# Kernel optimization log

Measured on AMD Instinct MI355X. Metric: run time of the kernel, lower is better.

## Reference

```python
import jax, jax.numpy as jnp
import numpy as np

N = 50000
E = 400000
NFEAT = 256
NHID = 64
HEADS = [4, 4, 4]
NCLASS = 121
NEG_SLOPE = 0.2


def gat_conv(h, W, al, ar, src, dst, H, D):
    # h: [N, F_in], W: [F_in, H*D], al/ar: [H, D]
    feat = (h @ W).reshape(N, H, D)                    # [N, H, D]
    el = jnp.sum(feat * al[None], axis=-1)             # [N, H]
    er = jnp.sum(feat * ar[None], axis=-1)             # [N, H]
    e = jax.nn.leaky_relu(el[src] + er[dst], NEG_SLOPE)  # [E, H]
    # edge softmax over incoming edges of each dst node
    m = jax.ops.segment_max(e, dst, num_segments=N)    # [N, H]
    ex = jnp.exp(e - m[dst])                           # [E, H]
    s = jax.ops.segment_sum(ex, dst, num_segments=N)   # [N, H]
    alpha = ex / s[dst]                                # [E, H]
    msg = alpha[..., None] * feat[src]                 # [E, H, D]
    return jax.ops.segment_sum(msg, dst, num_segments=N)  # [N, H, D]


def setup_inputs() -> dict:
    key = jax.random.key(0)
    ks = jax.random.split(key, 12)
    d = {
        "h": jax.random.normal(ks[0], (N, NFEAT), dtype=jnp.float32),
        "src": jax.random.randint(ks[1], (E,), 0, N),
        "dst": jax.random.randint(ks[2], (E,), 0, N),
        "W1": jax.random.normal(ks[3], (NFEAT, HEADS[0] * NHID), dtype=jnp.float32) * 0.05,
        "al1": jax.random.normal(ks[4], (HEADS[0], NHID), dtype=jnp.float32) * 0.1,
        "ar1": jax.random.normal(ks[5], (HEADS[0], NHID), dtype=jnp.float32) * 0.1,
        "W2": jax.random.normal(ks[6], (HEADS[0] * NHID, HEADS[1] * NHID), dtype=jnp.float32) * 0.05,
        "al2": jax.random.normal(ks[7], (HEADS[1], NHID), dtype=jnp.float32) * 0.1,
        "ar2": jax.random.normal(ks[8], (HEADS[1], NHID), dtype=jnp.float32) * 0.1,
        "W3": jax.random.normal(ks[9], (HEADS[1] * NHID, HEADS[2] * NCLASS), dtype=jnp.float32) * 0.05,
        "al3": jax.random.normal(ks[10], (HEADS[2], NCLASS), dtype=jnp.float32) * 0.1,
        "ar3": jax.random.normal(ks[11], (HEADS[2], NCLASS), dtype=jnp.float32) * 0.1,
    }
    return d


def reference(h, src, dst, W1, al1, ar1, W2, al2, ar2, W3, al3, ar3):
    # layer 1: [N, H0, NHID] -> flatten -> ELU (norm='none', drop=0, residual='none')
    x = gat_conv(h, W1, al1, ar1, src, dst, HEADS[0], NHID).reshape(N, -1)
    x = jax.nn.elu(x)
    # layer 2
    x = gat_conv(x, W2, al2, ar2, src, dst, HEADS[1], NHID).reshape(N, -1)
    x = jax.nn.elu(x)
    # output layer: mean over heads
    x = gat_conv(x, W3, al3, ar3, src, dst, HEADS[2], NCLASS).mean(axis=1)
    return x
```

## Files before the change

kernel.cpp:

```cpp
#include <hip/hip_runtime.h>
#include <cstddef>

#define NN 50000
#define NE 400000
#define NH 4
#define NC 121
#define MAXSLOT 600000

typedef __attribute__((ext_vector_type(8))) short short8;
typedef __attribute__((ext_vector_type(4))) float f32x4;
typedef __attribute__((ext_vector_type(2))) float f32x2;

static __device__ __forceinline__ unsigned short f2bf(float f) {
    unsigned u = __float_as_uint(f);
    u += 0x7fffu + ((u >> 16) & 1u);
    return (unsigned short)(u >> 16);
}
static __device__ __forceinline__ float bf2f(unsigned short u) {
    return __uint_as_float(((unsigned)u) << 16);
}
static __device__ __forceinline__ f32x2 bfpair(unsigned u) {
    f32x2 r;
    r.x = __uint_as_float(u << 16);
    r.y = __uint_as_float(u & 0xffff0000u);
    return r;
}
static __device__ __forceinline__ void load_lds16(const unsigned short* g, unsigned short* l) {
    __builtin_amdgcn_global_load_lds(
        (const __attribute__((address_space(1))) unsigned*)g,
        (__attribute__((address_space(3))) unsigned*)l, 16, 0, 0);
}

#define PREP_X    3200000
#define PREP_BT1  (PREP_X + 65536)
#define PREP_BT2  (PREP_BT1 + 65536)
#define PREP_CAT  (PREP_BT2 + 131072)
#define PREP_WV   (PREP_CAT + 2048)
__global__ __launch_bounds__(256) void prep_k(const float* __restrict__ h,
                                              const float* __restrict__ W1,
                                              const float* __restrict__ W2,
                                              const float* __restrict__ W3,
                                              const float* __restrict__ al3,
                                              const float* __restrict__ ar3,
                                              unsigned short* __restrict__ h_bf,
                                              unsigned short* __restrict__ BT1,
                                              unsigned short* __restrict__ BT2,
                                              unsigned short* __restrict__ BTcat,
                                              float* __restrict__ wl3,
                                              float* __restrict__ wr3) {
    int i = blockIdx.x * blockDim.x + threadIdx.x;
    if (i < PREP_X) {
        float4 v = *(const float4*)&h[(size_t)i * 4];
        ushort4 o;
        o.x = f2bf(v.x); o.y = f2bf(v.y); o.z = f2bf(v.z); o.w = f2bf(v.w);
        *(ushort4*)&h_bf[(size_t)i * 4] = o;
    } else if (i < PREP_BT1) {
        int j = i - PREP_X;
        int n = j >> 8, k = j & 255;
        BT1[j] = f2bf(W1[(size_t)k * 256 + n]);
    } else if (i < PREP_BT2) {
        int j = i - PREP_BT1;
        int n = j >> 8, k = j & 255;
        BT2[j] = f2bf(W2[(size_t)k * 256 + n]);
    } else if (i < PREP_CAT) {
        int j = i - PREP_BT2;
        int c = j >> 10, kk = j & 1023;
        int hh = kk >> 8, k = kk & 255;
        float v = (c < NC) ? 0.25f * W3[(size_t)k * 484 + hh * NC + c] : 0.f;
        BTcat[j] = f2bf(v);
    } else if (i < PREP_WV) {
        int j = (i - PREP_CAT) & 1023;
        int sel = (i - PREP_CAT) >> 10;
        int hh = j >> 8, k = j & 255;
        const float* a = sel ? ar3 : al3;
        const float* wrow = W3 + (size_t)k * 484 + hh * NC;
        const float* arow = a + hh * NC;
        float s = 0.f;
        for (int d = 0; d < NC; ++d) s += wrow[d] * arow[d];
        if (sel) wr3[j] = s; else wl3[j] = s;
    }
}

__global__ __launch_bounds__(256) void gemm_bf16(const unsigned short* __restrict__ A,
                                                 const unsigned short* __restrict__ BT,
                                                 float* __restrict__ Cf,
                                                 unsigned short* __restrict__ Cb,
                                                 const float* __restrict__ al,
                                                 const float* __restrict__ ar,
                                                 float* __restrict__ el,
                                                 float* __restrict__ er,
                                                 int M, int Nout, int K) {
    __shared__ __align__(16) unsigned short Alds[128 * 32];
    __shared__ __align__(16) unsigned short Blds[128 * 32];
    const int tid = threadIdx.x;
    const int wave = tid >> 6;
    const int lane = tid & 63;
    const int quad = lane >> 4;
    const int ml = lane & 15;
    const int m0 = blockIdx.x * 128;
    const int n0 = blockIdx.y * 128;
    const int wm0 = (wave >> 1) * 64;
    const int wn0 = (wave & 1) * 64;

    const unsigned short* Ab = A + (size_t)(m0 + wave * 16 + (lane >> 2)) * K + (lane & 3) * 8;
    const unsigned short* Bb = BT + (size_t)(n0 + wave * 16 + (lane >> 2)) * K + (lane & 3) * 8;
    unsigned short* AldsW = Alds + wave * 512;
    unsigned short* BldsW = Blds + wave * 512;

    f32x4 acc[4][4] = {};

    for (int k0 = 0; k0 < K; k0 += 32) {
        #pragma unroll
        for (int p = 0; p < 2; ++p) {
            load_lds16(Ab + (size_t)(p * 64) * K + k0, AldsW + p * 2048);
            load_lds16(Bb + (size_t)(p * 64) * K + k0, BldsW + p * 2048);
        }
        __syncthreads();

        short8 af[4], bf[4];
        #pragma unroll
        for (int i = 0; i < 4; ++i)
            af[i] = *(const short8*)&Alds[(wm0 + i * 16 + ml) * 32 + quad * 8];
        #pragma unroll
        for (int j = 0; j < 4; ++j)
            bf[j] = *(const short8*)&Blds[(wn0 + j * 16 + ml) * 32 + quad * 8];
        #pragma unroll
        for (int i = 0; i < 4; ++i)
            #pragma unroll
            for (int j = 0; j < 4; ++j)
                acc[i][j] = __builtin_amdgcn_mfma_f32_16x16x32_bf16(af[i], bf[j], acc[i][j], 0, 0, 0);
        __syncthreads();
    }

    #pragma unroll
    for (int i = 0; i < 4; ++i) {
        #pragma unroll
        for (int reg = 0; reg < 4; ++reg) {
            int m = m0 + wm0 + i * 16 + quad * 4 + reg;
            if (m >= M) continue;
            #pragma unroll
            for (int j = 0; j < 4; ++j) {
                int n = n0 + wn0 + j * 16 + ml;
                if (n < Nout) {
                    if (Cb) Cb[(size_t)m * Nout + n] = f2bf(acc[i][j][reg]);
                    else    Cf[(size_t)m * Nout + n] = acc[i][j][reg];
                }
            }
        }
    }

    if (el) {
        int head = (n0 + wn0) >> 6;
        float alv[4], arv[4];
        #pragma unroll
        for (int j = 0; j < 4; ++j) {
            alv[j] = al[head * 64 + j * 16 + ml];
            arv[j] = ar[head * 64 + j * 16 + ml];
        }
        #pragma unroll
        for (int i = 0; i < 4; ++i) {
            #pragma unroll
            for (int reg = 0; reg < 4; ++reg) {
                float sl = 0.f, sr = 0.f;
                #pragma unroll
                for (int j = 0; j < 4; ++j) {
                    float v = acc[i][j][reg];
                    sl += v * alv[j];
                    sr += v * arv[j];
                }
                #pragma unroll
                for (int off = 1; off < 16; off <<= 1) {
                    sl += __shfl_xor(sl, off);
                    sr += __shfl_xor(sr, off);
                }
                int m = m0 + wm0 + i * 16 + quad * 4 + reg;
                if (ml == 0 && m < M) {
                    el[m * 4 + head] = sl;
                    er[m * 4 + head] = sr;
                }
            }
        }
    }
}

__global__ __launch_bounds__(256) void hist_k(const int* __restrict__ dst, int* __restrict__ deg) {
    int e = blockIdx.x * blockDim.x + threadIdx.x;
    if (e < NE) atomicAdd(&deg[dst[e]], 1);
}

__global__ __launch_bounds__(256) void scan1(const int* __restrict__ deg,
                                             int* __restrict__ excl,
                                             int* __restrict__ partials) {
    __shared__ int sh[256];
    int i = blockIdx.x * 256 + threadIdx.x;
    int v = (i < NN) ? ((deg[i] + 3) & ~3) : 0;
    sh[threadIdx.x] = v;
    __syncthreads();
    for (int off = 1; off < 256; off <<= 1) {
        int t = (threadIdx.x >= off) ? sh[threadIdx.x - off] : 0;
        __syncthreads();
        sh[threadIdx.x] += t;
        __syncthreads();
    }
    if (i < NN) excl[i] = sh[threadIdx.x] - v;
    if (threadIdx.x == 255) partials[blockIdx.x] = sh[255];
}

__global__ __launch_bounds__(256) void scan2(int* __restrict__ partials, int nb) {
    __shared__ int sh[256];
    int t = threadIdx.x;
    int v = (t < nb) ? partials[t] : 0;
    sh[t] = v;
    __syncthreads();
    for (int off = 1; off < 256; off <<= 1) {
        int x = (t >= off) ? sh[t - off] : 0;
        __syncthreads();
        sh[t] += x;
        __syncthreads();
    }
    if (t < nb) partials[t] = sh[t] - v;
}

__global__ __launch_bounds__(256) void scan3(const int* __restrict__ excl,
                                             const int* __restrict__ partials,
                                             int* __restrict__ rowptr) {
    int i = blockIdx.x * 256 + threadIdx.x;
    if (i < NN) rowptr[i] = excl[i] + partials[blockIdx.x];
}

__global__ __launch_bounds__(256) void scatter_k(const int* __restrict__ src,
                                                 const int* __restrict__ dst,
                                                 const int* __restrict__ rowptr,
                                                 int* __restrict__ cursor,
                                                 int* __restrict__ ssrc,
                                                 int* __restrict__ sdst) {
    int e = blockIdx.x * blockDim.x + threadIdx.x;
    if (e >= NE) return;
    int d = dst[e];
    int p = atomicAdd(&cursor[d], 1);
    int pos = rowptr[d] + p;
    ssrc[pos] = src[e] << 9;
    sdst[pos] = d;
}

__global__ __launch_bounds__(256) void edgew_k(const int* __restrict__ ssrc,
                                               const int* __restrict__ sdst,
                                               const float* __restrict__ el,
                                               const float* __restrict__ er,
                                               float* __restrict__ wcsr) {
    int i = blockIdx.x * blockDim.x + threadIdx.x;
    if (i >= MAXSLOT) return;
    int d = sdst[i];
    float w0 = 0.f, w1 = 0.f, w2 = 0.f, w3 = 0.f;
    if (d >= 0) {
        int su = ssrc[i];
        float4 e_l = *(const float4*)((const char*)el + (su >> 5));
        float4 e_r = *(const float4*)&er[d * 4];
        float v0 = e_l.x + e_r.x; v0 = fmaxf(v0, 0.2f * v0);
        float v1 = e_l.y + e_r.y; v1 = fmaxf(v1, 0.2f * v1);
        float v2 = e_l.z + e_r.z; v2 = fmaxf(v2, 0.2f * v2);
        float v3 = e_l.w + e_r.w; v3 = fmaxf(v3, 0.2f * v3);
        w0 = __expf(v0); w1 = __expf(v1); w2 = __expf(v2); w3 = __expf(v3);
    }
    wcsr[0 * MAXSLOT + i] = w0;
    wcsr[1 * MAXSLOT + i] = w1;
    wcsr[2 * MAXSLOT + i] = w2;
    wcsr[3 * MAXSLOT + i] = w3;
}

__global__ __launch_bounds__(256) void agg256(const int* __restrict__ rowptr,
                                              const int* __restrict__ deg,
                                              const int* __restrict__ ssrc,
                                              const float* __restrict__ wcsr,
                                              const unsigned short* __restrict__ feat,
                                              unsigned short* __restrict__ ybf,
                                              const float* __restrict__ wl3,
                                              const float* __restrict__ wr3,
                                              float* __restrict__ el3,
                                              float* __restrict__ er3) {
    int wid = (blockIdx.x * blockDim.x + threadIdx.x) >> 6;
    int lane = threadIdx.x & 63;
    if (wid >= NN) return;
    int n = wid;
    int start = rowptr[n];
    int cnt4 = (deg[n] + 3) & ~3;
    int head = lane >> 4;
    const float* wch = wcsr + (size_t)head * MAXSLOT;
    const char* fbase = (const char*)feat + lane * 8;
    f32x2 a01 = {0.f, 0.f}, a23 = {0.f, 0.f};
    float ssum = 0.f;
    for (int k = 0; k < cnt4; k += 4) {
        int4 sv = *(const int4*)&ssrc[start + k];
        float4 w4 = *(const float4*)&wch[start + k];
        uint2 u0 = *(const uint2*)(fbase + sv.x);
        uint2 u1 = *(const uint2*)(fbase + sv.y);
        uint2 u2 = *(const uint2*)(fbase + sv.z);
        uint2 u3 = *(const uint2*)(fbase + sv.w);
        ssum += (w4.x + w4.y) + (w4.z + w4.w);
        a01 += w4.x * bfpair(u0.x); a23 += w4.x * bfpair(u0.y);
        a01 += w4.y * bfpair(u1.x); a23 += w4.y * bfpair(u1.y);
        a01 += w4.z * bfpair(u2.x); a23 += w4.z * bfpair(u2.y);
        a01 += w4.w * bfpair(u3.x); a23 += w4.w * bfpair(u3.y);
    }
    float inv = ssum > 0.f ? 1.0f / ssum : 0.f;
    float r0 = a01.x * inv, r1 = a01.y * inv, r2 = a23.x * inv, r3 = a23.y * inv;
    r0 = r0 > 0.f ? r0 : (__expf(r0) - 1.f);
    r1 = r1 > 0.f ? r1 : (__expf(r1) - 1.f);
    r2 = r2 > 0.f ? r2 : (__expf(r2) - 1.f);
    r3 = r3 > 0.f ? r3 : (__expf(r3) - 1.f);
    ushort4 o;
    o.x = f2bf(r0); o.y = f2bf(r1); o.z = f2bf(r2); o.w = f2bf(r3);
    *(ushort4*)&ybf[(size_t)n * 256 + lane * 4] = o;

    if (wl3) {
        float sl[4], sr[4];
        #pragma unroll
        for (int h = 0; h < 4; ++h) {
            float4 a4 = *(const float4*)&wl3[h * 256 + lane * 4];
            float4 b4 = *(const float4*)&wr3[h * 256 + lane * 4];
            sl[h] = r0 * a4.x + r1 * a4.y + r2 * a4.z + r3 * a4.w;
            sr[h] = r0 * b4.x + r1 * b4.y + r2 * b4.z + r3 * b4.w;
        }
        #pragma unroll
        for (int off = 32; off; off >>= 1) {
            #pragma unroll
            for (int h = 0; h < 4; ++h) {
                sl[h] += __shfl_xor(sl[h], off);
                sr[h] += __shfl_xor(sr[h], off);
            }
        }
        if (lane == 0) {
            #pragma unroll
            for (int h = 0; h < 4; ++h) {
                el3[n * 4 + h] = sl[h];
                er3[n * 4 + h] = sr[h];
            }
        }
    }
}

__global__ __launch_bounds__(256) void agg3(const int* __restrict__ rowptr,
                                            const int* __restrict__ deg,
                                            const int* __restrict__ ssrc,
                                            const float* __restrict__ wcsr,
                                            const unsigned short* __restrict__ x,
                                            unsigned short* __restrict__ xagg) {
    int wid = (blockIdx.x * blockDim.x + threadIdx.x) >> 6;
    int lane = threadIdx.x & 63;
    if (wid >= NN) return;
    int n = wid;
    int start = rowptr[n];
    int cnt4 = (deg[n] + 3) & ~3;
    const char* xbase = (const char*)x + lane * 8;
    f32x2 accA[4] = {}, accB[4] = {};
    float ssum[4] = {};
    for (int k = 0; k < cnt4; k += 4) {
        int4 sv = *(const int4*)&ssrc[start + k];
        float4 w0 = *(const float4*)&wcsr[0 * MAXSLOT + start + k];
        float4 w1 = *(const float4*)&wcsr[1 * MAXSLOT + start + k];
        float4 w2 = *(const float4*)&wcsr[2 * MAXSLOT + start + k];
        float4 w3 = *(const float4*)&wcsr[3 * MAXSLOT + start + k];
        uint2 u0 = *(const uint2*)(xbase + sv.x);
        uint2 u1 = *(const uint2*)(xbase + sv.y);
        uint2 u2 = *(const uint2*)(xbase + sv.z);
        uint2 u3 = *(const uint2*)(xbase + sv.w);
        ssum[0] += (w0.x + w0.y) + (w0.z + w0.w);
        ssum[1] += (w1.x + w1.y) + (w1.z + w1.w);
        ssum[2] += (w2.x + w2.y) + (w2.z + w2.w);
        ssum[3] += (w3.x + w3.y) + (w3.z + w3.w);
        f32x2 fa = bfpair(u0.x), fA = bfpair(u0.y);
        f32x2 fb = bfpair(u1.x), fB = bfpair(u1.y);
        f32x2 fc = bfpair(u2.x), fC = bfpair(u2.y);
        f32x2 fd = bfpair(u3.x), fD = bfpair(u3.y);
        accA[0] += w0.x * fa + w0.y * fb + w0.z * fc + w0.w * fd;
        accB[0] += w0.x * fA + w0.y * fB + w0.z * fC + w0.w * fD;
        accA[1] += w1.x * fa + w1.y * fb + w1.z * fc + w1.w * fd;
        accB[1] += w1.x * fA + w1.y * fB + w1.z * fC + w1.w * fD;
        accA[2] += w2.x * fa + w2.y * fb + w2.z * fc + w2.w * fd;
        accB[2] += w2.x * fA + w2.y * fB + w2.z * fC + w2.w * fD;
        accA[3] += w3.x * fa + w3.y * fb + w3.z * fc + w3.w * fd;
        accB[3] += w3.x * fA + w3.y * fB + w3.z * fC + w3.w * fD;
    }
    #pragma unroll
    for (int h = 0; h < 4; ++h) {
        float inv = ssum[h] > 0.f ? 1.f / ssum[h] : 0.f;
        ushort4 o;
        o.x = f2bf(accA[h].x * inv); o.y = f2bf(accA[h].y * inv);
        o.z = f2bf(accB[h].x * inv); o.w = f2bf(accB[h].y * inv);
        *(ushort4*)&xagg[(size_t)n * 1024 + h * 256 + lane * 4] = o;
    }
}

extern "C" void kernel_launch(void* const* d_in, const int* in_sizes, int n_in,
                              void* d_out, int out_size, void* d_ws, size_t ws_size,
                              hipStream_t stream) {
    const float* h   = (const float*)d_in[0];
    const int*   src = (const int*)d_in[1];
    const int*   dst = (const int*)d_in[2];
    const float* W1  = (const float*)d_in[3];
    const float* al1 = (const float*)d_in[4];
    const float* ar1 = (const float*)d_in[5];
    const float* W2  = (const float*)d_in[6];
    const float* al2 = (const float*)d_in[7];
    const float* ar2 = (const float*)d_in[8];
    const float* W3  = (const float*)d_in[9];
    const float* al3 = (const float*)d_in[10];
    const float* ar3 = (const float*)d_in[11];
    float* out = (float*)d_out;

    float* ws = (float*)d_ws;
    unsigned short* x_bf    = (unsigned short*)ws;
    unsigned short* h_bf    = (unsigned short*)(ws + 6400000);
    unsigned short* feat_bf = (unsigned short*)(ws + 12800000);
    unsigned short* xagg    = (unsigned short*)(ws + 6400000);
    float* el  = ws + 32000000;
    float* er  = ws + 32200000;
    float* wl3 = ws + 32400000;
    float* wr3 = ws + 32401024;
    unsigned short* BT1   = (unsigned short*)(ws + 32402048);
    unsigned short* BT2   = (unsigned short*)(ws + 32434816);
    unsigned short* BTcat = (unsigned short*)(ws + 32467584);
    float* wcsr = ws + 32533120;
    int* ibase  = (int*)(ws + 34933120);
    int* deg      = ibase;
    int* cursor   = ibase + 50000;
    int* excl     = ibase + 100000;
    int* partials = ibase + 150000;
    int* rowptr   = ibase + 150256;
    int* ssrc     = ibase + 200256;
    int* sdst     = ibase + 800256;

    const int NB = (NN + 255) / 256;
    const int SLOT_BLOCKS = (MAXSLOT + 255) / 256;

    hipMemsetAsync(deg, 0, 2 * NN * sizeof(int), stream);
    hipMemsetAsync(ssrc, 0, MAXSLOT * sizeof(int), stream);
    hipMemsetAsync(sdst, 0xFF, MAXSLOT * sizeof(int), stream);
    hist_k<<<(NE + 255) / 256, 256, 0, stream>>>(dst, deg);
    scan1<<<NB, 256, 0, stream>>>(deg, excl, partials);
    scan2<<<1, 256, 0, stream>>>(partials, NB);
    scan3<<<NB, 256, 0, stream>>>(excl, partials, rowptr);
    scatter_k<<<(NE + 255) / 256, 256, 0, stream>>>(src, dst, rowptr, cursor, ssrc, sdst);

    prep_k<<<(PREP_WV + 255) / 256, 256, 0, stream>>>(h, W1, W2, W3, al3, ar3,
                                                      h_bf, BT1, BT2, BTcat, wl3, wr3);

    dim3 g256((NN + 127) / 128, 2);
    dim3 gOut((NN + 127) / 128, 1);
    const int WAVE_BLOCKS = (NN * 64 + 255) / 256;

    gemm_bf16<<<g256, 256, 0, stream>>>(h_bf, BT1, nullptr, feat_bf, al1, ar1, el, er, NN, 256, 256);
    edgew_k<<<SLOT_BLOCKS, 256, 0, stream>>>(ssrc, sdst, el, er, wcsr);
    agg256<<<WAVE_BLOCKS, 256, 0, stream>>>(rowptr, deg, ssrc, wcsr, feat_bf, x_bf,
                                            nullptr, nullptr, nullptr, nullptr);

    gemm_bf16<<<g256, 256, 0, stream>>>(x_bf, BT2, nullptr, feat_bf, al2, ar2, el, er, NN, 256, 256);
    edgew_k<<<SLOT_BLOCKS, 256, 0, stream>>>(ssrc, sdst, el, er, wcsr);
    agg256<<<WAVE_BLOCKS, 256, 0, stream>>>(rowptr, deg, ssrc, wcsr, feat_bf, x_bf,
                                            wl3, wr3, el, er);

    edgew_k<<<SLOT_BLOCKS, 256, 0, stream>>>(ssrc, sdst, el, er, wcsr);
    agg3<<<WAVE_BLOCKS, 256, 0, stream>>>(rowptr, deg, ssrc, wcsr, x_bf, xagg);
    gemm_bf16<<<gOut, 256, 0, stream>>>(xagg, BTcat, out, nullptr, nullptr, nullptr, nullptr, nullptr, NN, NC, 1024);
}
```

Before: 413.3 us.

## Fuse edge-weight computation into layer aggregation and degree histogram into prep

Drops the separate edgew_k pass for layers 1 and 2. Each agg256 wave now gathers el[src] per edge, applies leaky-relu and exp inline, and masks padded slots, so the per-edge weight array is no longer written and then read back. The degree histogram is folded into prep_k as extra threads, which removes one launch. Layer 3's attention logits go to separate el2/er2 buffers so the in-place el/er update stays safe. The cost is redundant exp and gather work: all 16 lanes of a head recompute the same edge weights.

```diff
diff --git a/kernel.cpp b/kernel.cpp
--- a/kernel.cpp
+++ b/kernel.cpp
@@ -36,18 +36,21 @@
 #define PREP_BT2  (PREP_BT1 + 65536)
 #define PREP_CAT  (PREP_BT2 + 131072)
 #define PREP_WV   (PREP_CAT + 2048)
+#define PREP_END  (PREP_WV + NE)
 __global__ __launch_bounds__(256) void prep_k(const float* __restrict__ h,
                                               const float* __restrict__ W1,
                                               const float* __restrict__ W2,
                                               const float* __restrict__ W3,
                                               const float* __restrict__ al3,
                                               const float* __restrict__ ar3,
+                                              const int* __restrict__ dst,
                                               unsigned short* __restrict__ h_bf,
                                               unsigned short* __restrict__ BT1,
                                               unsigned short* __restrict__ BT2,
                                               unsigned short* __restrict__ BTcat,
                                               float* __restrict__ wl3,
-                                              float* __restrict__ wr3) {
+                                              float* __restrict__ wr3,
+                                              int* __restrict__ deg) {
     int i = blockIdx.x * blockDim.x + threadIdx.x;
     if (i < PREP_X) {
         float4 v = *(const float4*)&h[(size_t)i * 4];
@@ -78,6 +81,8 @@
         float s = 0.f;
         for (int d = 0; d < NC; ++d) s += wrow[d] * arow[d];
         if (sel) wr3[j] = s; else wl3[j] = s;
+    } else if (i < PREP_END) {
+        atomicAdd(&deg[dst[i - PREP_WV]], 1);
     }
 }
 
@@ -183,11 +188,6 @@
     }
 }
 
-__global__ __launch_bounds__(256) void hist_k(const int* __restrict__ dst, int* __restrict__ deg) {
-    int e = blockIdx.x * blockDim.x + threadIdx.x;
-    if (e < NE) atomicAdd(&deg[dst[e]], 1);
-}
-
 __global__ __launch_bounds__(256) void scan1(const int* __restrict__ deg,
                                              int* __restrict__ excl,
                                              int* __restrict__ partials) {
@@ -271,7 +271,8 @@
 __global__ __launch_bounds__(256) void agg256(const int* __restrict__ rowptr,
                                               const int* __restrict__ deg,
                                               const int* __restrict__ ssrc,
-                                              const float* __restrict__ wcsr,
+                                              const float* __restrict__ el,
+                                              const float* __restrict__ er,
                                               const unsigned short* __restrict__ feat,
                                               unsigned short* __restrict__ ybf,
                                               const float* __restrict__ wl3,
@@ -283,24 +284,37 @@
     if (wid >= NN) return;
     int n = wid;
     int start = rowptr[n];
-    int cnt4 = (deg[n] + 3) & ~3;
+    int cnt = deg[n];
+    int cnt4 = (cnt + 3) & ~3;
     int head = lane >> 4;
-    const float* wch = wcsr + (size_t)head * MAXSLOT;
+    float ern = er[n * 4 + head];
+    const char* elb = (const char*)el + head * 4;
     const char* fbase = (const char*)feat + lane * 8;
     f32x2 a01 = {0.f, 0.f}, a23 = {0.f, 0.f};
     float ssum = 0.f;
     for (int k = 0; k < cnt4; k += 4) {
         int4 sv = *(const int4*)&ssrc[start + k];
-        float4 w4 = *(const float4*)&wch[start + k];
+        float e0 = *(const float*)(elb + (sv.x >> 5));
+        float e1 = *(const float*)(elb + (sv.y >> 5));
+        float e2 = *(const float*)(elb + (sv.z >> 5));
+        float e3 = *(const float*)(elb + (sv.w >> 5));
+        float v0 = e0 + ern; v0 = fmaxf(v0, 0.2f * v0);
+        float v1 = e1 + ern; v1 = fmaxf(v1, 0.2f * v1);
+        float v2 = e2 + ern; v2 = fmaxf(v2, 0.2f * v2);
+        float v3 = e3 + ern; v3 = fmaxf(v3, 0.2f * v3);
+        float w0 = (k + 0 < cnt) ? __expf(v0) : 0.f;
+        float w1 = (k + 1 < cnt) ? __expf(v1) : 0.f;
+        float w2 = (k + 2 < cnt) ? __expf(v2) : 0.f;
+        float w3 = (k + 3 < cnt) ? __expf(v3) : 0.f;
         uint2 u0 = *(const uint2*)(fbase + sv.x);
         uint2 u1 = *(const uint2*)(fbase + sv.y);
         uint2 u2 = *(const uint2*)(fbase + sv.z);
         uint2 u3 = *(const uint2*)(fbase + sv.w);
-        ssum += (w4.x + w4.y) + (w4.z + w4.w);
-        a01 += w4.x * bfpair(u0.x); a23 += w4.x * bfpair(u0.y);
-        a01 += w4.y * bfpair(u1.x); a23 += w4.y * bfpair(u1.y);
-        a01 += w4.z * bfpair(u2.x); a23 += w4.z * bfpair(u2.y);
-        a01 += w4.w * bfpair(u3.x); a23 += w4.w * bfpair(u3.y);
+        ssum += (w0 + w1) + (w2 + w3);
+        a01 += w0 * bfpair(u0.x); a23 += w0 * bfpair(u0.y);
+        a01 += w1 * bfpair(u1.x); a23 += w1 * bfpair(u1.y);
+        a01 += w2 * bfpair(u2.x); a23 += w2 * bfpair(u2.y);
+        a01 += w3 * bfpair(u3.x); a23 += w3 * bfpair(u3.y);
     }
     float inv = ssum > 0.f ? 1.0f / ssum : 0.f;
     float r0 = a01.x * inv, r1 = a01.y * inv, r2 = a23.x * inv, r3 = a23.y * inv;
@@ -429,6 +443,8 @@
     int* rowptr   = ibase + 150256;
     int* ssrc     = ibase + 200256;
     int* sdst     = ibase + 800256;
+    float* el2 = ws + 36333376;
+    float* er2 = ws + 36533376;
 
     const int NB = (NN + 255) / 256;
     const int SLOT_BLOCKS = (MAXSLOT + 255) / 256;
@@ -436,30 +452,28 @@
     hipMemsetAsync(deg, 0, 2 * NN * sizeof(int), stream);
     hipMemsetAsync(ssrc, 0, MAXSLOT * sizeof(int), stream);
     hipMemsetAsync(sdst, 0xFF, MAXSLOT * sizeof(int), stream);
-    hist_k<<<(NE + 255) / 256, 256, 0, stream>>>(dst, deg);
+
+    prep_k<<<(PREP_END + 255) / 256, 256, 0, stream>>>(h, W1, W2, W3, al3, ar3, dst,
+                                                       h_bf, BT1, BT2, BTcat, wl3, wr3, deg);
+
     scan1<<<NB, 256, 0, stream>>>(deg, excl, partials);
     scan2<<<1, 256, 0, stream>>>(partials, NB);
     scan3<<<NB, 256, 0, stream>>>(excl, partials, rowptr);
     scatter_k<<<(NE + 255) / 256, 256, 0, stream>>>(src, dst, rowptr, cursor, ssrc, sdst);
 
-    prep_k<<<(PREP_WV + 255) / 256, 256, 0, stream>>>(h, W1, W2, W3, al3, ar3,
-                                                      h_bf, BT1, BT2, BTcat, wl3, wr3);
-
     dim3 g256((NN + 127) / 128, 2);
     dim3 gOut((NN + 127) / 128, 1);
     const int WAVE_BLOCKS = (NN * 64 + 255) / 256;
 
     gemm_bf16<<<g256, 256, 0, stream>>>(h_bf, BT1, nullptr, feat_bf, al1, ar1, el, er, NN, 256, 256);
-    edgew_k<<<SLOT_BLOCKS, 256, 0, stream>>>(ssrc, sdst, el, er, wcsr);
-    agg256<<<WAVE_BLOCKS, 256, 0, stream>>>(rowptr, deg, ssrc, wcsr, feat_bf, x_bf,
+    agg256<<<WAVE_BLOCKS, 256, 0, stream>>>(rowptr, deg, ssrc, el, er, feat_bf, x_bf,
                                             nullptr, nullptr, nullptr, nullptr);
 
     gemm_bf16<<<g256, 256, 0, stream>>>(x_bf, BT2, nullptr, feat_bf, al2, ar2, el, er, NN, 256, 256);
-    edgew_k<<<SLOT_BLOCKS, 256, 0, stream>>>(ssrc, sdst, el, er, wcsr);
-    agg256<<<WAVE_BLOCKS, 256, 0, stream>>>(rowptr, deg, ssrc, wcsr, feat_bf, x_bf,
-                                            wl3, wr3, el, er);
-
-    edgew_k<<<SLOT_BLOCKS, 256, 0, stream>>>(ssrc, sdst, el, er, wcsr);
+    agg256<<<WAVE_BLOCKS, 256, 0, stream>>>(rowptr, deg, ssrc, el, er, feat_bf, x_bf,
+                                            wl3, wr3, el2, er2);
+
+    edgew_k<<<SLOT_BLOCKS, 256, 0, stream>>>(ssrc, sdst, el2, er2, wcsr);
     agg3<<<WAVE_BLOCKS, 256, 0, stream>>>(rowptr, deg, ssrc, wcsr, x_bf, xagg);
     gemm_bf16<<<gOut, 256, 0, stream>>>(xagg, BTcat, out, nullptr, nullptr, nullptr, nullptr, nullptr, NN, NC, 1024);
 }
```

Result: faster. 403.3 us (-2.4%).
